# Optimization experiments

Hardware: AMD Instinct MI355X
Metric: run time of the kernel (lower is better)

Reference implementation:

```python
import jax, jax.numpy as jnp
import numpy as np

B, N, E_PER = 32, 2048, 16384
DIN, H = 128, 128
RATIO = 0.3


def setup_inputs() -> dict:
    key = jax.random.key(0)
    ks = jax.random.split(key, 16)
    s_in = 1.0 / np.sqrt(DIN)
    s_h = 1.0 / np.sqrt(H)
    inp = {
        "x": jax.random.normal(ks[0], (B * N, DIN), dtype=jnp.float32),
        "edge_src": jax.random.randint(ks[1], (B, E_PER), 0, N, dtype=jnp.int32),
        "edge_dst": jax.random.randint(ks[2], (B, E_PER), 0, N, dtype=jnp.int32),
        # SAGEConv layer 1: lin_l (neighbor agg, with bias), lin_r (root, no bias)
        "Wl1": jax.random.normal(ks[3], (H, DIN), dtype=jnp.float32) * s_in,
        "bl1": jnp.zeros((H,), dtype=jnp.float32),
        "Wr1": jax.random.normal(ks[4], (H, DIN), dtype=jnp.float32) * s_in,
        # SAGEConv layer 2
        "Wl2": jax.random.normal(ks[5], (H, H), dtype=jnp.float32) * s_h,
        "bl2": jnp.zeros((H,), dtype=jnp.float32),
        "Wr2": jax.random.normal(ks[6], (H, H), dtype=jnp.float32) * s_h,
        # TopKPooling score weight
        "pool_w": jax.random.normal(ks[7], (H,), dtype=jnp.float32) * s_h,
        # classifier MLP
        "Wc1": jax.random.normal(ks[8], (H, H), dtype=jnp.float32) * s_h,
        "bc1": jnp.zeros((H,), dtype=jnp.float32),
        "Wc2": jax.random.normal(ks[9], (1, H), dtype=jnp.float32) * s_h,
        "bc2": jnp.zeros((1,), dtype=jnp.float32),
    }
    return inp


def _sage_conv(x, src, dst, n_total, Wl, bl, Wr):
    # mean-aggregate neighbor messages: msg flows src -> dst
    msg = x[src]                                                   # [E, D] gather
    agg = jax.ops.segment_sum(msg, dst, num_segments=n_total)      # [Nt, D]
    deg = jax.ops.segment_sum(jnp.ones_like(dst, dtype=x.dtype), dst,
                              num_segments=n_total)
    agg = agg / jnp.maximum(deg, 1.0)[:, None]
    return agg @ Wl.T + bl + x @ Wr.T


def _forward(x, edge_src, edge_dst, Wl1, bl1, Wr1, Wl2, bl2, Wr2,
             pool_w, Wc1, bc1, Wc2, bc2):
    n_total = x.shape[0]
    # offset per-graph node ids into the disjoint-union batch
    off = (jnp.arange(B, dtype=edge_src.dtype) * N)[:, None]
    src = (edge_src + off).reshape(-1)
    dst = (edge_dst + off).reshape(-1)

    x = jax.nn.relu(_sage_conv(x, src, dst, n_total, Wl1, bl1, Wr1))
    x = jax.nn.relu(_sage_conv(x, src, dst, n_total, Wl2, bl2, Wr2))

    # TopKPooling: score = tanh(x . w / ||w||); keep top ceil(ratio*N) per graph
    score = jnp.tanh(x @ pool_w / jnp.linalg.norm(pool_w))         # [Nt]
    k = int(np.ceil(RATIO * N))                                    # 615
    vals, idx = jax.lax.top_k(score.reshape(B, N), k)              # [B, k]
    xg = x.reshape(B, N, -1)
    x_sel = jnp.take_along_axis(xg, idx[..., None], axis=1)        # [B, k, H]
    x_sel = x_sel * vals[..., None]                                # gate by score

    # global mean pool over kept nodes, then MLP classifier
    emb = x_sel.mean(axis=1)                                       # [B, H]
    h = jax.nn.relu(emb @ Wc1.T + bc1)
    return (h @ Wc2.T + bc2).squeeze(-1)                           # [B]


def reference(x, edge_src, edge_dst, Wl1, bl1, Wr1, Wl2, bl2, Wr2,
              pool_w, Wc1, bc1, Wc2, bc2):
    return _forward(x, edge_src, edge_dst, Wl1, bl1, Wr1, Wl2, bl2, Wr2,
                    pool_w, Wc1, bc1, Wc2, bc2)
```

## Files before the change

kernel.cpp:

```cpp
#include <hip/hip_runtime.h>
#include <stdint.h>
#include <math.h>

#define NB    32
#define NNODE 2048
#define NT    (NB*NNODE)
#define EPB   16384
#define ETOT  (NB*EPB)
#define DF    128
#define KSEL  615
#define EMAX  512

typedef __attribute__((ext_vector_type(8))) short bf16x8;
typedef __attribute__((ext_vector_type(4))) float f32x4;

__device__ __forceinline__ unsigned short f2bf(float f){
  uint32_t u = __float_as_uint(f);
  u += 0x7FFFu + ((u>>16)&1u);
  return (unsigned short)(u>>16);
}
__device__ __forceinline__ void split2(float f, unsigned short& hi, unsigned short& lo){
  unsigned short h = f2bf(f);
  float fh = __uint_as_float(((uint32_t)h)<<16);
  hi = h;
  lo = f2bf(f - fh);
}
__device__ __forceinline__ uint32_t f2mono(float f){
  uint32_t u = __float_as_uint(f);
  return (u & 0x80000000u) ? ~u : (u | 0x80000000u);
}
__device__ __forceinline__ float mono2f(uint32_t m){
  uint32_t u = (m & 0x80000000u) ? (m ^ 0x80000000u) : ~m;
  return __uint_as_float(u);
}

__global__ void k_deg(const int* __restrict__ edst, uint32_t* __restrict__ deg){
  int e = blockIdx.x*256 + threadIdx.x;
  int g = e >> 14;
  atomicAdd(&deg[g*NNODE + edst[e]], 1u);
}

__global__ __launch_bounds__(1024) void k_scan1(const uint32_t* __restrict__ deg,
                        uint32_t* __restrict__ rowptr, uint32_t* __restrict__ bsum){
  __shared__ uint32_t sh[1024];
  int t = threadIdx.x; int base = blockIdx.x*1024;
  uint32_t v = deg[base+t];
  sh[t] = v;
  for (int off=1; off<1024; off<<=1){
    __syncthreads();
    uint32_t a = (t>=off) ? sh[t-off] : 0u;
    __syncthreads();
    sh[t] += a;
  }
  rowptr[base+t] = sh[t] - v;
  if (t==1023) bsum[blockIdx.x] = sh[1023];
}

__global__ void k_scan2(uint32_t* __restrict__ bsum){
  __shared__ uint32_t sh[64];
  int t = threadIdx.x;
  uint32_t v = bsum[t]; sh[t] = v;
  for (int off=1; off<64; off<<=1){
    __syncthreads();
    uint32_t a = (t>=off) ? sh[t-off] : 0u;
    __syncthreads();
    sh[t] += a;
  }
  bsum[t] = sh[t] - v;
}

__global__ __launch_bounds__(1024) void k_scan3(uint32_t* __restrict__ rowptr,
                                                const uint32_t* __restrict__ bsum){
  int i = blockIdx.x*1024 + threadIdx.x;
  rowptr[i] += bsum[i>>10];
  if (i==0) rowptr[NT] = ETOT;
}

__global__ void k_scatter(const int* __restrict__ esrc, const int* __restrict__ edst,
                          const uint32_t* __restrict__ rowptr, uint32_t* __restrict__ deg,
                          int* __restrict__ col){
  int e = blockIdx.x*256 + threadIdx.x;
  int g = e >> 14;
  int d = g*NNODE + edst[e];
  int s = g*NNODE + esrc[e];
  uint32_t old = atomicSub(&deg[d], 1u);
  col[rowptr[d] + old - 1u] = s;
}

__global__ void k_packB(const float* __restrict__ Wl, const float* __restrict__ Wr,
                        unsigned short* __restrict__ Bpk){
  int t = blockIdx.x*256 + threadIdx.x;
  int lane = t & 63;
  int ct   = (t>>6) & 7;
  int ks   = (t>>9) & 7;
  int c  = ct*16 + (lane & 15);
  int k0 = ks*32 + ((lane>>4)<<3);
  size_t base = ((size_t)((ks*8+ct)*2)*64 + lane)*8;
  #pragma unroll
  for (int j=0;j<8;++j){
    int k = k0 + j;
    float v = (k < DF) ? Wl[c*DF + k] : Wr[c*DF + (k-DF)];
    unsigned short h, l; split2(v, h, l);
    Bpk[base + j]       = h;
    Bpk[base + 512 + j] = l;
  }
}

template<int LAYER>
__global__ __launch_bounds__(128, 4) void k_sage(
    const float* __restrict__ Xin, const uint32_t* __restrict__ rowptr,
    const int* __restrict__ col, const unsigned short* __restrict__ Bpk,
    const float* __restrict__ bias, float* __restrict__ OUT,
    const float* __restrict__ pw, float* __restrict__ scores)
{
  __shared__ float smemA[32][132];
  __shared__ int lcol[EMAX];
  __shared__ uint32_t lrp[33];

  const int t = threadIdx.x;
  const int g = blockIdx.x & 31, jb = blockIdx.x >> 5;
  const int rowBase = g*NNODE + jb*32;

  if (t < 33) lrp[t] = rowptr[rowBase + t];
  const uint32_t e0 = rowptr[rowBase];
  const int ecnt = (int)(rowptr[rowBase + 32] - e0);
  for (int i=t; i<ecnt && i<EMAX; i+=128) lcol[i] = col[e0+i];
  __syncthreads();

  {
    const int grp = t >> 5, c = t & 31;
    const float4* X4 = (const float4*)Xin;
    auto gather = [&](auto colAt){
      for (int n=grp; n<32; n+=4){
        uint32_t b = lrp[n] - e0, e = lrp[n+1] - e0;
        float ax=0.f, ay=0.f, az=0.f, aw=0.f;
        uint32_t k = b;
        for (; k+8<=e; k+=8){
          int s0=colAt(k),  s1=colAt(k+1), s2=colAt(k+2), s3=colAt(k+3),
              s4=colAt(k+4),s5=colAt(k+5), s6=colAt(k+6), s7=colAt(k+7);
          float4 v0=X4[(size_t)s0*32+c], v1=X4[(size_t)s1*32+c],
                 v2=X4[(size_t)s2*32+c], v3=X4[(size_t)s3*32+c],
                 v4=X4[(size_t)s4*32+c], v5=X4[(size_t)s5*32+c],
                 v6=X4[(size_t)s6*32+c], v7=X4[(size_t)s7*32+c];
          ax += ((v0.x+v1.x)+(v2.x+v3.x)) + ((v4.x+v5.x)+(v6.x+v7.x));
          ay += ((v0.y+v1.y)+(v2.y+v3.y)) + ((v4.y+v5.y)+(v6.y+v7.y));
          az += ((v0.z+v1.z)+(v2.z+v3.z)) + ((v4.z+v5.z)+(v6.z+v7.z));
          aw += ((v0.w+v1.w)+(v2.w+v3.w)) + ((v4.w+v5.w)+(v6.w+v7.w));
        }
        for (; k+4<=e; k+=4){
          int s0=colAt(k), s1=colAt(k+1), s2=colAt(k+2), s3=colAt(k+3);
          float4 v0=X4[(size_t)s0*32+c], v1=X4[(size_t)s1*32+c],
                 v2=X4[(size_t)s2*32+c], v3=X4[(size_t)s3*32+c];
          ax += (v0.x+v1.x)+(v2.x+v3.x);
          ay += (v0.y+v1.y)+(v2.y+v3.y);
          az += (v0.z+v1.z)+(v2.z+v3.z);
          aw += (v0.w+v1.w)+(v2.w+v3.w);
        }
        for (; k<e; ++k){
          float4 v = X4[(size_t)colAt(k)*32+c];
          ax+=v.x; ay+=v.y; az+=v.z; aw+=v.w;
        }
        float invd = 1.0f / (float)((e>b)?(e-b):1u);
        *(float4*)&smemA[n][4*c] = make_float4(ax*invd, ay*invd, az*invd, aw*invd);
      }
    };
    if (ecnt <= EMAX) gather([&](uint32_t k){ return lcol[k]; });
    else              gather([&](uint32_t k){ return col[e0+k]; });
  }
  __syncthreads();

  const int l = t & 63, wid = t >> 6;
  const int q = l >> 4, c16 = l & 15;
  const int arow = rowBase + wid*16 + c16;

  f32x4 acc[8];
  #pragma unroll
  for (int ct=0; ct<8; ++ct) acc[ct] = (f32x4){0.f,0.f,0.f,0.f};

  #pragma unroll
  for (int ks=0; ks<8; ++ks){
    float4 A0, A1;
    if (ks < 4){
      const float* s = &smemA[wid*16 + c16][ks*32 + q*8];
      A0 = *(const float4*)s; A1 = *(const float4*)(s+4);
    } else {
      const float* s = Xin + (size_t)arow*DF + (ks-4)*32 + q*8;
      A0 = *(const float4*)s; A1 = *(const float4*)(s+4);
    }
    float v[8] = {A0.x,A0.y,A0.z,A0.w,A1.x,A1.y,A1.z,A1.w};
    bf16x8 ahi, alo;
    #pragma unroll
    for (int j=0;j<8;++j){
      unsigned short h, lo_; split2(v[j], h, lo_);
      ahi[j] = (short)h; alo[j] = (short)lo_;
    }
    const unsigned short* bp = Bpk + (size_t)ks*8192 + l*8;
    #pragma unroll
    for (int ct=0; ct<8; ++ct){
      bf16x8 bhi = *(const bf16x8*)(bp + ct*1024);
      bf16x8 blo = *(const bf16x8*)(bp + ct*1024 + 512);
      acc[ct] = __builtin_amdgcn_mfma_f32_16x16x32_bf16(ahi, bhi, acc[ct], 0,0,0);
      acc[ct] = __builtin_amdgcn_mfma_f32_16x16x32_bf16(ahi, blo, acc[ct], 0,0,0);
      acc[ct] = __builtin_amdgcn_mfma_f32_16x16x32_bf16(alo, bhi, acc[ct], 0,0,0);
    }
  }

  const int rowOut = rowBase + wid*16;
  if constexpr (LAYER==1){
    #pragma unroll
    for (int ct=0; ct<8; ++ct){
      int c = ct*16 + c16;
      float bv = bias[c];
      #pragma unroll
      for (int r=0; r<4; ++r){
        int grow = rowOut + q*4 + r;
        OUT[(size_t)grow*DF + c] = fmaxf(acc[ct][r] + bv, 0.f);
      }
    }
  } else {
    float ov[8][4];
    float pwv[8];
    float n2 = 0.f;
    #pragma unroll
    for (int ct=0; ct<8; ++ct){ pwv[ct] = pw[ct*16 + c16]; n2 += pwv[ct]*pwv[ct]; }
    n2 += __shfl_xor(n2,8,16); n2 += __shfl_xor(n2,4,16);
    n2 += __shfl_xor(n2,2,16); n2 += __shfl_xor(n2,1,16);
    float nrm = sqrtf(n2);
    #pragma unroll
    for (int ct=0; ct<8; ++ct){
      int c = ct*16 + c16;
      float bv = bias[c];
      #pragma unroll
      for (int r=0; r<4; ++r){
        int grow = rowOut + q*4 + r;
        float o = fmaxf(acc[ct][r] + bv, 0.f);
        OUT[(size_t)grow*DF + c] = o;
        ov[ct][r] = o;
      }
    }
    #pragma unroll
    for (int r=0; r<4; ++r){
      float p = 0.f;
      #pragma unroll
      for (int ct=0; ct<8; ++ct) p += ov[ct][r]*pwv[ct];
      p += __shfl_xor(p,8,16); p += __shfl_xor(p,4,16);
      p += __shfl_xor(p,2,16); p += __shfl_xor(p,1,16);
      if (c16 == 0) scores[rowOut + q*4 + r] = tanhf(p/nrm);
    }
  }
}

__global__ __launch_bounds__(1024) void k_topk(
    const float* __restrict__ scores, const float* __restrict__ H,
    const float* __restrict__ Wc1, const float* __restrict__ bc1,
    const float* __restrict__ Wc2, const float* __restrict__ bc2,
    float* __restrict__ out)
{
  __shared__ uint32_t keys[NNODE];
  __shared__ uint32_t hist[64];
  __shared__ uint32_t wsum[16];
  __shared__ uint32_t sh_b, sh_rank, sh_cnt;
  __shared__ unsigned short selidx[KSEL+1];
  __shared__ float selval[KSEL+1];
  __shared__ float part[8*DF];
  __shared__ float emb[DF];
  __shared__ float hred[DF];

  const int t = threadIdx.x; const int b = blockIdx.x;
  const int lane = t & 63, wid = t >> 6;
  const float* sc = scores + b*NNODE;

  for (int i=t; i<NNODE; i+=1024) keys[i] = f2mono(sc[i]);
  __syncthreads();

  uint32_t prefix = 0, prefmask = 0, rank = KSEL, cntT = 0;
  #pragma unroll
  for (int lev=0; lev<6; ++lev){
    const int shift = (lev<5) ? (26 - 6*lev) : 0;
    const uint32_t bmask = (lev<5) ? 63u : 3u;
    if (t < 64) hist[t] = 0;
    __syncthreads();
    for (int i=t; i<NNODE; i+=1024){
      uint32_t k = keys[i];
      if ((k & prefmask) == prefix) atomicAdd(&hist[(k>>shift)&bmask], 1u);
    }
    __syncthreads();
    if (t < 64){
      uint32_t x = hist[t];
      #pragma unroll
      for (int off=1; off<64; off<<=1){
        uint32_t y = __shfl_down(x, off, 64);
        if (t + off < 64) x += y;
      }
      uint32_t above = __shfl_down(x, 1, 64);
      if (t == 63) above = 0;
      if (above < rank && rank <= x){
        sh_b = (uint32_t)t; sh_rank = rank - above; sh_cnt = x - above;
      }
    }
    __syncthreads();
    prefix |= (sh_b << shift);
    prefmask |= (bmask << shift);
    rank = sh_rank; cntT = sh_cnt;
    __syncthreads();
  }
  const uint32_t T = prefix;
  const uint32_t m = rank;

  uint32_t k0 = keys[2*t], k1 = keys[2*t+1];
  uint32_t eq0 = (k0 == T), eq1 = (k1 == T);
  uint32_t eqr0 = 0, eqr1 = 0;

  if (m != cntT){
    uint32_t v = eq0 + eq1, x = v;
    #pragma unroll
    for (int off=1; off<64; off<<=1){
      uint32_t y = __shfl_up(x, off, 64);
      if (lane >= off) x += y;
    }
    if (lane == 63) wsum[wid] = x;
    __syncthreads();
    if (wid == 0){
      uint32_t s = (lane < 16) ? wsum[lane] : 0;
      #pragma unroll
      for (int off=1; off<16; off<<=1){
        uint32_t y = __shfl_up(s, off, 64);
        if (lane >= off) s += y;
      }
      if (lane < 16) wsum[lane] = s;
    }
    __syncthreads();
    uint32_t excl = (wid ? wsum[wid-1] : 0) + x - v;
    eqr0 = excl; eqr1 = excl + eq0;
    __syncthreads();
  }

  uint32_t sel0 = (k0 > T) || (eq0 && eqr0 < m);
  uint32_t sel1 = (k1 > T) || (eq1 && eqr1 < m);
  {
    uint32_t v = sel0 + sel1, x = v;
    #pragma unroll
    for (int off=1; off<64; off<<=1){
      uint32_t y = __shfl_up(x, off, 64);
      if (lane >= off) x += y;
    }
    if (lane == 63) wsum[wid] = x;
    __syncthreads();
    if (wid == 0){
      uint32_t s = (lane < 16) ? wsum[lane] : 0;
      #pragma unroll
      for (int off=1; off<16; off<<=1){
        uint32_t y = __shfl_up(s, off, 64);
        if (lane >= off) s += y;
      }
      if (lane < 16) wsum[lane] = s;
    }
    __syncthreads();
    uint32_t excl = (wid ? wsum[wid-1] : 0) + x - v;
    if (sel0){ selidx[excl] = (unsigned short)(2*t);   selval[excl] = mono2f(k0); }
    if (sel1){ selidx[excl+sel0] = (unsigned short)(2*t+1); selval[excl+sel0] = mono2f(k1); }
  }
  __syncthreads();

  const int pg = t >> 7, f = t & (DF-1);
  const float* Hb = H + (size_t)b*NNODE*DF;
  float accv = 0.f;
  int s2 = pg;
  for (; s2+24 < KSEL; s2 += 32){
    int i0=selidx[s2], i1=selidx[s2+8], i2=selidx[s2+16], i3=selidx[s2+24];
    float w0=selval[s2], w1=selval[s2+8], w2=selval[s2+16], w3=selval[s2+24];
    float v0=Hb[(size_t)i0*DF+f], v1=Hb[(size_t)i1*DF+f],
          v2=Hb[(size_t)i2*DF+f], v3=Hb[(size_t)i3*DF+f];
    accv += w0*v0 + w1*v1 + w2*v2 + w3*v3;
  }
  for (; s2<KSEL; s2+=8) accv += selval[s2]*Hb[(size_t)selidx[s2]*DF+f];
  part[pg*DF + f] = accv;
  __syncthreads();
  if (t < DF){
    float e = 0.f;
    for (int g2=0; g2<8; ++g2) e += part[g2*DF + t];
    emb[t] = e / (float)KSEL;
  }
  __syncthreads();
  if (t < DF){
    float hv = bc1[t];
    const float* wr = Wc1 + t*DF;
    for (int f2=0; f2<DF; ++f2) hv = fmaf(emb[f2], wr[f2], hv);
    hred[t] = fmaxf(hv, 0.f) * Wc2[t];
  }
  __syncthreads();
  if (t == 0){
    float o = bc2[0];
    for (int c2=0; c2<DF; ++c2) o += hred[c2];
    out[b] = o;
  }
}

extern "C" void kernel_launch(void* const* d_in, const int* in_sizes, int n_in,
                              void* d_out, int out_size, void* d_ws, size_t ws_size,
                              hipStream_t stream)
{
  (void)in_sizes; (void)n_in; (void)out_size; (void)ws_size;
  const float* x   = (const float*)d_in[0];
  const int* esrc  = (const int*)d_in[1];
  const int* edst  = (const int*)d_in[2];
  const float* Wl1 = (const float*)d_in[3];
  const float* bl1 = (const float*)d_in[4];
  const float* Wr1 = (const float*)d_in[5];
  const float* Wl2 = (const float*)d_in[6];
  const float* bl2 = (const float*)d_in[7];
  const float* Wr2 = (const float*)d_in[8];
  const float* pw  = (const float*)d_in[9];
  const float* Wc1 = (const float*)d_in[10];
  const float* bc1 = (const float*)d_in[11];
  const float* Wc2 = (const float*)d_in[12];
  const float* bc2 = (const float*)d_in[13];
  float* out = (float*)d_out;

  char* ws = (char*)d_ws;
  float*    H1     = (float*)   (ws + 0);
  float*    H2     = (float*)   (ws + 33554432);
  uint32_t* deg    = (uint32_t*)(ws + 67108864);
  uint32_t* rowptr = (uint32_t*)(ws + 67371008);
  int*      col    = (int*)     (ws + 67633408);
  float*    scores = (float*)   (ws + 69730560);
  uint32_t* bsum   = (uint32_t*)(ws + 69992704);
  unsigned short* Bpk = (unsigned short*)(ws + 69992960);

  hipMemsetAsync(deg, 0, NT*sizeof(uint32_t), stream);

  k_deg    <<<ETOT/256, 256, 0, stream>>>(edst, deg);
  k_scan1  <<<64, 1024, 0, stream>>>(deg, rowptr, bsum);
  k_scan2  <<<1, 64, 0, stream>>>(bsum);
  k_scan3  <<<64, 1024, 0, stream>>>(rowptr, bsum);
  k_scatter<<<ETOT/256, 256, 0, stream>>>(esrc, edst, rowptr, deg, col);

  k_packB<<<16, 256, 0, stream>>>(Wl1, Wr1, Bpk);
  k_packB<<<16, 256, 0, stream>>>(Wl2, Wr2, Bpk + 65536);

  k_sage<1><<<NT/32, 128, 0, stream>>>(x,  rowptr, col, Bpk,         bl1,
                                       H1, nullptr, nullptr);
  k_sage<2><<<NT/32, 128, 0, stream>>>(H1, rowptr, col, Bpk + 65536, bl2,
                                       H2, pw, scores);

  k_topk<<<NB, 1024, 0, stream>>>(scores, H2, Wc1, bc1, Wc2, bc2, out);
}
```

Baseline: 161.3 us.

## Double SAGE block to 256 threads, split output columns across waves, merge packB launches

```diff
diff --git a/kernel.cpp b/kernel.cpp
--- a/kernel.cpp
+++ b/kernel.cpp
@@ -87,9 +87,15 @@
   col[rowptr[d] + old - 1u] = s;
 }
 
-__global__ void k_packB(const float* __restrict__ Wl, const float* __restrict__ Wr,
+__global__ void k_packB(const float* __restrict__ Wl1, const float* __restrict__ Wr1,
+                        const float* __restrict__ Wl2, const float* __restrict__ Wr2,
                         unsigned short* __restrict__ Bpk){
-  int t = blockIdx.x*256 + threadIdx.x;
+  int tt = blockIdx.x*256 + threadIdx.x;
+  int layer = tt >> 12;
+  int t = tt & 4095;
+  const float* Wl = layer ? Wl2 : Wl1;
+  const float* Wr = layer ? Wr2 : Wr1;
+  unsigned short* B = Bpk + (size_t)layer*65536;
   int lane = t & 63;
   int ct   = (t>>6) & 7;
   int ks   = (t>>9) & 7;
@@ -101,13 +107,13 @@
     int k = k0 + j;
     float v = (k < DF) ? Wl[c*DF + k] : Wr[c*DF + (k-DF)];
     unsigned short h, l; split2(v, h, l);
-    Bpk[base + j]       = h;
-    Bpk[base + 512 + j] = l;
+    B[base + j]       = h;
+    B[base + 512 + j] = l;
   }
 }
 
 template<int LAYER>
-__global__ __launch_bounds__(128, 4) void k_sage(
+__global__ __launch_bounds__(256, 4) void k_sage(
     const float* __restrict__ Xin, const uint32_t* __restrict__ rowptr,
     const int* __restrict__ col, const unsigned short* __restrict__ Bpk,
     const float* __restrict__ bias, float* __restrict__ OUT,
@@ -116,6 +122,8 @@
   __shared__ float smemA[32][132];
   __shared__ int lcol[EMAX];
   __shared__ uint32_t lrp[33];
+  __shared__ float sp_p[32][2];
+  __shared__ float sp_n2[2];
 
   const int t = threadIdx.x;
   const int g = blockIdx.x & 31, jb = blockIdx.x >> 5;
@@ -124,14 +132,27 @@
   if (t < 33) lrp[t] = rowptr[rowBase + t];
   const uint32_t e0 = rowptr[rowBase];
   const int ecnt = (int)(rowptr[rowBase + 32] - e0);
-  for (int i=t; i<ecnt && i<EMAX; i+=128) lcol[i] = col[e0+i];
+  for (int i=t; i<ecnt && i<EMAX; i+=256) lcol[i] = col[e0+i];
+
+  const int l = t & 63, wid = t >> 6;
+  const int q = l >> 4, c16 = l & 15;
+  const int rhalf = wid & 1, cthalf = wid >> 1;
+  const int arow = rowBase + rhalf*16 + c16;
+
+  float4 own[8];
+  #pragma unroll
+  for (int ks4=0; ks4<4; ++ks4){
+    const float* s = Xin + (size_t)arow*DF + ks4*32 + q*8;
+    own[ks4*2]   = *(const float4*)s;
+    own[ks4*2+1] = *(const float4*)(s+4);
+  }
   __syncthreads();
 
   {
     const int grp = t >> 5, c = t & 31;
     const float4* X4 = (const float4*)Xin;
     auto gather = [&](auto colAt){
-      for (int n=grp; n<32; n+=4){
+      for (int n=grp; n<32; n+=8){
         uint32_t b = lrp[n] - e0, e = lrp[n+1] - e0;
         float ax=0.f, ay=0.f, az=0.f, aw=0.f;
         uint32_t k = b;
@@ -169,23 +190,18 @@
   }
   __syncthreads();
 
-  const int l = t & 63, wid = t >> 6;
-  const int q = l >> 4, c16 = l & 15;
-  const int arow = rowBase + wid*16 + c16;
-
-  f32x4 acc[8];
+  f32x4 acc[4];
   #pragma unroll
-  for (int ct=0; ct<8; ++ct) acc[ct] = (f32x4){0.f,0.f,0.f,0.f};
+  for (int ct=0; ct<4; ++ct) acc[ct] = (f32x4){0.f,0.f,0.f,0.f};
 
   #pragma unroll
   for (int ks=0; ks<8; ++ks){
     float4 A0, A1;
     if (ks < 4){
-      const float* s = &smemA[wid*16 + c16][ks*32 + q*8];
+      const float* s = &smemA[rhalf*16 + c16][ks*32 + q*8];
       A0 = *(const float4*)s; A1 = *(const float4*)(s+4);
     } else {
-      const float* s = Xin + (size_t)arow*DF + (ks-4)*32 + q*8;
-      A0 = *(const float4*)s; A1 = *(const float4*)(s+4);
+      A0 = own[(ks-4)*2]; A1 = own[(ks-4)*2+1];
     }
     float v[8] = {A0.x,A0.y,A0.z,A0.w,A1.x,A1.y,A1.z,A1.w};
     bf16x8 ahi, alo;
@@ -194,9 +210,9 @@
       unsigned short h, lo_; split2(v[j], h, lo_);
       ahi[j] = (short)h; alo[j] = (short)lo_;
     }
-    const unsigned short* bp = Bpk + (size_t)ks*8192 + l*8;
-    #pragma unroll
-    for (int ct=0; ct<8; ++ct){
+    const unsigned short* bp = Bpk + (size_t)ks*8192 + (size_t)cthalf*4096 + l*8;
+    #pragma unroll
+    for (int ct=0; ct<4; ++ct){
       bf16x8 bhi = *(const bf16x8*)(bp + ct*1024);
       bf16x8 blo = *(const bf16x8*)(bp + ct*1024 + 512);
       acc[ct] = __builtin_amdgcn_mfma_f32_16x16x32_bf16(ahi, bhi, acc[ct], 0,0,0);
@@ -205,11 +221,11 @@
     }
   }
 
-  const int rowOut = rowBase + wid*16;
+  const int rowOut = rowBase + rhalf*16;
   if constexpr (LAYER==1){
     #pragma unroll
-    for (int ct=0; ct<8; ++ct){
-      int c = ct*16 + c16;
+    for (int ct=0; ct<4; ++ct){
+      int c = cthalf*64 + ct*16 + c16;
       float bv = bias[c];
       #pragma unroll
       for (int r=0; r<4; ++r){
@@ -218,17 +234,20 @@
       }
     }
   } else {
-    float ov[8][4];
-    float pwv[8];
+    float ov[4][4];
+    float pwv[4];
     float n2 = 0.f;
     #pragma unroll
-    for (int ct=0; ct<8; ++ct){ pwv[ct] = pw[ct*16 + c16]; n2 += pwv[ct]*pwv[ct]; }
+    for (int ct=0; ct<4; ++ct){
+      pwv[ct] = pw[cthalf*64 + ct*16 + c16];
+      n2 += pwv[ct]*pwv[ct];
+    }
     n2 += __shfl_xor(n2,8,16); n2 += __shfl_xor(n2,4,16);
     n2 += __shfl_xor(n2,2,16); n2 += __shfl_xor(n2,1,16);
-    float nrm = sqrtf(n2);
-    #pragma unroll
-    for (int ct=0; ct<8; ++ct){
-      int c = ct*16 + c16;
+    if (l == 0) sp_n2[cthalf] = n2;
+    #pragma unroll
+    for (int ct=0; ct<4; ++ct){
+      int c = cthalf*64 + ct*16 + c16;
       float bv = bias[c];
       #pragma unroll
       for (int r=0; r<4; ++r){
@@ -242,10 +261,16 @@
     for (int r=0; r<4; ++r){
       float p = 0.f;
       #pragma unroll
-      for (int ct=0; ct<8; ++ct) p += ov[ct][r]*pwv[ct];
+      for (int ct=0; ct<4; ++ct) p += ov[ct][r]*pwv[ct];
       p += __shfl_xor(p,8,16); p += __shfl_xor(p,4,16);
       p += __shfl_xor(p,2,16); p += __shfl_xor(p,1,16);
-      if (c16 == 0) scores[rowOut + q*4 + r] = tanhf(p/nrm);
+      if (c16 == 0) sp_p[rhalf*16 + q*4 + r][cthalf] = p;
+    }
+    __syncthreads();
+    if (t < 32){
+      float p = sp_p[t][0] + sp_p[t][1];
+      float nrm = sqrtf(sp_n2[0] + sp_n2[1]);
+      scores[rowBase + t] = tanhf(p/nrm);
     }
   }
 }
@@ -435,12 +460,11 @@
   k_scan3  <<<64, 1024, 0, stream>>>(rowptr, bsum);
   k_scatter<<<ETOT/256, 256, 0, stream>>>(esrc, edst, rowptr, deg, col);
 
-  k_packB<<<16, 256, 0, stream>>>(Wl1, Wr1, Bpk);
-  k_packB<<<16, 256, 0, stream>>>(Wl2, Wr2, Bpk + 65536);
-
-  k_sage<1><<<NT/32, 128, 0, stream>>>(x,  rowptr, col, Bpk,         bl1,
+  k_packB<<<32, 256, 0, stream>>>(Wl1, Wr1, Wl2, Wr2, Bpk);
+
+  k_sage<1><<<NT/32, 256, 0, stream>>>(x,  rowptr, col, Bpk,         bl1,
                                        H1, nullptr, nullptr);
-  k_sage<2><<<NT/32, 128, 0, stream>>>(H1, rowptr, col, Bpk + 65536, bl2,
+  k_sage<2><<<NT/32, 256, 0, stream>>>(H1, rowptr, col, Bpk + 65536, bl2,
                                        H2, pw, scores);
 
   k_topk<<<NB, 1024, 0, stream>>>(scores, H2, Wc1, bc1, Wc2, bc2, out);
```

Measured after the change: 168.3 us. 1.04x slower.

## Fuse CSR build and weight packing into one per-graph LDS kernel

Applied to the files above, without the earlier changes.

```diff
diff --git a/kernel.cpp b/kernel.cpp
--- a/kernel.cpp
+++ b/kernel.cpp
@@ -33,76 +33,92 @@
   uint32_t u = (m & 0x80000000u) ? (m ^ 0x80000000u) : ~m;
   return __uint_as_float(u);
 }
-
-__global__ void k_deg(const int* __restrict__ edst, uint32_t* __restrict__ deg){
-  int e = blockIdx.x*256 + threadIdx.x;
-  int g = e >> 14;
-  atomicAdd(&deg[g*NNODE + edst[e]], 1u);
-}
-
-__global__ __launch_bounds__(1024) void k_scan1(const uint32_t* __restrict__ deg,
-                        uint32_t* __restrict__ rowptr, uint32_t* __restrict__ bsum){
-  __shared__ uint32_t sh[1024];
-  int t = threadIdx.x; int base = blockIdx.x*1024;
-  uint32_t v = deg[base+t];
-  sh[t] = v;
-  for (int off=1; off<1024; off<<=1){
-    __syncthreads();
-    uint32_t a = (t>=off) ? sh[t-off] : 0u;
-    __syncthreads();
-    sh[t] += a;
-  }
-  rowptr[base+t] = sh[t] - v;
-  if (t==1023) bsum[blockIdx.x] = sh[1023];
-}
-
-__global__ void k_scan2(uint32_t* __restrict__ bsum){
-  __shared__ uint32_t sh[64];
-  int t = threadIdx.x;
-  uint32_t v = bsum[t]; sh[t] = v;
-  for (int off=1; off<64; off<<=1){
-    __syncthreads();
-    uint32_t a = (t>=off) ? sh[t-off] : 0u;
-    __syncthreads();
-    sh[t] += a;
-  }
-  bsum[t] = sh[t] - v;
-}
-
-__global__ __launch_bounds__(1024) void k_scan3(uint32_t* __restrict__ rowptr,
-                                                const uint32_t* __restrict__ bsum){
-  int i = blockIdx.x*1024 + threadIdx.x;
-  rowptr[i] += bsum[i>>10];
-  if (i==0) rowptr[NT] = ETOT;
-}
-
-__global__ void k_scatter(const int* __restrict__ esrc, const int* __restrict__ edst,
-                          const uint32_t* __restrict__ rowptr, uint32_t* __restrict__ deg,
-                          int* __restrict__ col){
-  int e = blockIdx.x*256 + threadIdx.x;
-  int g = e >> 14;
-  int d = g*NNODE + edst[e];
-  int s = g*NNODE + esrc[e];
-  uint32_t old = atomicSub(&deg[d], 1u);
-  col[rowptr[d] + old - 1u] = s;
-}
-
-__global__ void k_packB(const float* __restrict__ Wl, const float* __restrict__ Wr,
-                        unsigned short* __restrict__ Bpk){
-  int t = blockIdx.x*256 + threadIdx.x;
-  int lane = t & 63;
-  int ct   = (t>>6) & 7;
-  int ks   = (t>>9) & 7;
-  int c  = ct*16 + (lane & 15);
-  int k0 = ks*32 + ((lane>>4)<<3);
-  size_t base = ((size_t)((ks*8+ct)*2)*64 + lane)*8;
-  #pragma unroll
-  for (int j=0;j<8;++j){
-    int k = k0 + j;
-    float v = (k < DF) ? Wl[c*DF + k] : Wr[c*DF + (k-DF)];
-    unsigned short h, l; split2(v, h, l);
-    Bpk[base + j]       = h;
-    Bpk[base + 512 + j] = l;
+__device__ __forceinline__ f32x4 ntload4(const float* p){
+  return __builtin_nontemporal_load((const f32x4*)p);
+}
+__device__ __forceinline__ void ntstore(float v, float* p){
+  __builtin_nontemporal_store(v, p);
+}
+
+__global__ __launch_bounds__(256) void k_prep(
+    const int* __restrict__ esrc, const int* __restrict__ edst,
+    const float* __restrict__ Wl1, const float* __restrict__ Wr1,
+    const float* __restrict__ Wl2, const float* __restrict__ Wr2,
+    uint32_t* __restrict__ rowptr, int* __restrict__ col,
+    unsigned short* __restrict__ Bpk)
+{
+  __shared__ uint32_t hist[NNODE];
+  __shared__ uint32_t wsum4[4];
+  const int t = threadIdx.x;
+  const int bid = blockIdx.x;
+
+  if (bid < NB){
+    const int g = bid;
+    const int lane = t & 63, wid = t >> 6;
+    for (int i=t; i<NNODE; i+=256) hist[i] = 0;
+    __syncthreads();
+    const int* ed = edst + g*EPB;
+    const int* es = esrc + g*EPB;
+    for (int e=t; e<EPB; e+=256) atomicAdd(&hist[ed[e]], 1u);
+    __syncthreads();
+    uint32_t v0,v1,v2,v3,v4,v5,v6,v7;
+    const int b8 = t*8;
+    v0=hist[b8+0]; v1=hist[b8+1]; v2=hist[b8+2]; v3=hist[b8+3];
+    v4=hist[b8+4]; v5=hist[b8+5]; v6=hist[b8+6]; v7=hist[b8+7];
+    uint32_t tsum = v0+v1+v2+v3+v4+v5+v6+v7;
+    uint32_t x = tsum;
+    #pragma unroll
+    for (int off=1; off<64; off<<=1){
+      uint32_t y = __shfl_up(x, off, 64);
+      if (lane >= off) x += y;
+    }
+    if (lane == 63) wsum4[wid] = x;
+    __syncthreads();
+    if (t == 0){
+      uint32_t a = 0;
+      #pragma unroll
+      for (int w=0; w<4; ++w){ uint32_t tmp=wsum4[w]; wsum4[w]=a; a+=tmp; }
+    }
+    __syncthreads();
+    uint32_t run = wsum4[wid] + x - tsum;
+    uint32_t* rp = rowptr + g*NNODE + b8;
+    uint32_t h;
+    h=v0; hist[b8+0]=run; rp[0]=g*EPB+run; run+=h;
+    h=v1; hist[b8+1]=run; rp[1]=g*EPB+run; run+=h;
+    h=v2; hist[b8+2]=run; rp[2]=g*EPB+run; run+=h;
+    h=v3; hist[b8+3]=run; rp[3]=g*EPB+run; run+=h;
+    h=v4; hist[b8+4]=run; rp[4]=g*EPB+run; run+=h;
+    h=v5; hist[b8+5]=run; rp[5]=g*EPB+run; run+=h;
+    h=v6; hist[b8+6]=run; rp[6]=g*EPB+run; run+=h;
+    h=v7; hist[b8+7]=run; rp[7]=g*EPB+run; run+=h;
+    if (g == 0 && t == 0) rowptr[NT] = ETOT;
+    __syncthreads();
+    for (int e=t; e<EPB; e+=256){
+      int d = ed[e];
+      uint32_t slot = atomicAdd(&hist[d], 1u);
+      col[g*EPB + slot] = g*NNODE + es[e];
+    }
+  } else {
+    int tt = (bid - NB)*256 + t;
+    int layer = tt >> 12;
+    int t2 = tt & 4095;
+    const float* Wl = layer ? Wl2 : Wl1;
+    const float* Wr = layer ? Wr2 : Wr1;
+    unsigned short* B = Bpk + (size_t)layer*65536;
+    int lane = t2 & 63;
+    int ct   = (t2>>6) & 7;
+    int ks   = (t2>>9) & 7;
+    int c  = ct*16 + (lane & 15);
+    int k0 = ks*32 + ((lane>>4)<<3);
+    size_t base = ((size_t)((ks*8+ct)*2)*64 + lane)*8;
+    #pragma unroll
+    for (int j=0;j<8;++j){
+      int k = k0 + j;
+      float v = (k < DF) ? Wl[c*DF + k] : Wr[c*DF + (k-DF)];
+      unsigned short h, l; split2(v, h, l);
+      B[base + j]       = h;
+      B[base + 512 + j] = l;
+    }
   }
 }
 
@@ -125,43 +141,46 @@
   const uint32_t e0 = rowptr[rowBase];
   const int ecnt = (int)(rowptr[rowBase + 32] - e0);
   for (int i=t; i<ecnt && i<EMAX; i+=128) lcol[i] = col[e0+i];
+
+  const int l = t & 63, wid = t >> 6;
+  const int q = l >> 4, c16 = l & 15;
+  const int arow = rowBase + wid*16 + c16;
+  f32x4 own[8];
+  #pragma unroll
+  for (int ks4=0; ks4<4; ++ks4){
+    const float* s = Xin + (size_t)arow*DF + ks4*32 + q*8;
+    own[ks4*2]   = ntload4(s);
+    own[ks4*2+1] = ntload4(s+4);
+  }
   __syncthreads();
 
   {
     const int grp = t >> 5, c = t & 31;
-    const float4* X4 = (const float4*)Xin;
     auto gather = [&](auto colAt){
       for (int n=grp; n<32; n+=4){
         uint32_t b = lrp[n] - e0, e = lrp[n+1] - e0;
-        float ax=0.f, ay=0.f, az=0.f, aw=0.f;
+        f32x4 a = {0.f,0.f,0.f,0.f};
         uint32_t k = b;
         for (; k+8<=e; k+=8){
           int s0=colAt(k),  s1=colAt(k+1), s2=colAt(k+2), s3=colAt(k+3),
               s4=colAt(k+4),s5=colAt(k+5), s6=colAt(k+6), s7=colAt(k+7);
-          float4 v0=X4[(size_t)s0*32+c], v1=X4[(size_t)s1*32+c],
-                 v2=X4[(size_t)s2*32+c], v3=X4[(size_t)s3*32+c],
-                 v4=X4[(size_t)s4*32+c], v5=X4[(size_t)s5*32+c],
-                 v6=X4[(size_t)s6*32+c], v7=X4[(size_t)s7*32+c];
-          ax += ((v0.x+v1.x)+(v2.x+v3.x)) + ((v4.x+v5.x)+(v6.x+v7.x));
-          ay += ((v0.y+v1.y)+(v2.y+v3.y)) + ((v4.y+v5.y)+(v6.y+v7.y));
-          az += ((v0.z+v1.z)+(v2.z+v3.z)) + ((v4.z+v5.z)+(v6.z+v7.z));
-          aw += ((v0.w+v1.w)+(v2.w+v3.w)) + ((v4.w+v5.w)+(v6.w+v7.w));
+          f32x4 v0=ntload4(Xin+(size_t)s0*DF+4*c), v1=ntload4(Xin+(size_t)s1*DF+4*c),
+                v2=ntload4(Xin+(size_t)s2*DF+4*c), v3=ntload4(Xin+(size_t)s3*DF+4*c),
+                v4=ntload4(Xin+(size_t)s4*DF+4*c), v5=ntload4(Xin+(size_t)s5*DF+4*c),
+                v6=ntload4(Xin+(size_t)s6*DF+4*c), v7=ntload4(Xin+(size_t)s7*DF+4*c);
+          a += ((v0+v1)+(v2+v3)) + ((v4+v5)+(v6+v7));
         }
         for (; k+4<=e; k+=4){
           int s0=colAt(k), s1=colAt(k+1), s2=colAt(k+2), s3=colAt(k+3);
-          float4 v0=X4[(size_t)s0*32+c], v1=X4[(size_t)s1*32+c],
-                 v2=X4[(size_t)s2*32+c], v3=X4[(size_t)s3*32+c];
-          ax += (v0.x+v1.x)+(v2.x+v3.x);
-          ay += (v0.y+v1.y)+(v2.y+v3.y);
-          az += (v0.z+v1.z)+(v2.z+v3.z);
-          aw += (v0.w+v1.w)+(v2.w+v3.w);
+          f32x4 v0=ntload4(Xin+(size_t)s0*DF+4*c), v1=ntload4(Xin+(size_t)s1*DF+4*c),
+                v2=ntload4(Xin+(size_t)s2*DF+4*c), v3=ntload4(Xin+(size_t)s3*DF+4*c);
+          a += (v0+v1)+(v2+v3);
         }
         for (; k<e; ++k){
-          float4 v = X4[(size_t)colAt(k)*32+c];
-          ax+=v.x; ay+=v.y; az+=v.z; aw+=v.w;
+          a += ntload4(Xin+(size_t)colAt(k)*DF+4*c);
         }
         float invd = 1.0f / (float)((e>b)?(e-b):1u);
-        *(float4*)&smemA[n][4*c] = make_float4(ax*invd, ay*invd, az*invd, aw*invd);
+        *(f32x4*)&smemA[n][4*c] = a * invd;
       }
     };
     if (ecnt <= EMAX) gather([&](uint32_t k){ return lcol[k]; });
@@ -169,23 +188,18 @@
   }
   __syncthreads();
 
-  const int l = t & 63, wid = t >> 6;
-  const int q = l >> 4, c16 = l & 15;
-  const int arow = rowBase + wid*16 + c16;
-
   f32x4 acc[8];
   #pragma unroll
   for (int ct=0; ct<8; ++ct) acc[ct] = (f32x4){0.f,0.f,0.f,0.f};
 
   #pragma unroll
   for (int ks=0; ks<8; ++ks){
-    float4 A0, A1;
+    f32x4 A0, A1;
     if (ks < 4){
       const float* s = &smemA[wid*16 + c16][ks*32 + q*8];
-      A0 = *(const float4*)s; A1 = *(const float4*)(s+4);
+      A0 = *(const f32x4*)s; A1 = *(const f32x4*)(s+4);
     } else {
-      const float* s = Xin + (size_t)arow*DF + (ks-4)*32 + q*8;
-      A0 = *(const float4*)s; A1 = *(const float4*)(s+4);
+      A0 = own[(ks-4)*2]; A1 = own[(ks-4)*2+1];
     }
     float v[8] = {A0.x,A0.y,A0.z,A0.w,A1.x,A1.y,A1.z,A1.w};
     bf16x8 ahi, alo;
@@ -214,7 +228,7 @@
       #pragma unroll
       for (int r=0; r<4; ++r){
         int grow = rowOut + q*4 + r;
-        OUT[(size_t)grow*DF + c] = fmaxf(acc[ct][r] + bv, 0.f);
+        ntstore(fmaxf(acc[ct][r] + bv, 0.f), &OUT[(size_t)grow*DF + c]);
       }
     }
   } else {
@@ -234,7 +248,7 @@
       for (int r=0; r<4; ++r){
         int grow = rowOut + q*4 + r;
         float o = fmaxf(acc[ct][r] + bv, 0.f);
-        OUT[(size_t)grow*DF + c] = o;
+        ntstore(o, &OUT[(size_t)grow*DF + c]);
         ov[ct][r] = o;
       }
     }
@@ -420,23 +434,13 @@
   char* ws = (char*)d_ws;
   float*    H1     = (float*)   (ws + 0);
   float*    H2     = (float*)   (ws + 33554432);
-  uint32_t* deg    = (uint32_t*)(ws + 67108864);
-  uint32_t* rowptr = (uint32_t*)(ws + 67371008);
-  int*      col    = (int*)     (ws + 67633408);
-  float*    scores = (float*)   (ws + 69730560);
-  uint32_t* bsum   = (uint32_t*)(ws + 69992704);
-  unsigned short* Bpk = (unsigned short*)(ws + 69992960);
-
-  hipMemsetAsync(deg, 0, NT*sizeof(uint32_t), stream);
-
-  k_deg    <<<ETOT/256, 256, 0, stream>>>(edst, deg);
-  k_scan1  <<<64, 1024, 0, stream>>>(deg, rowptr, bsum);
-  k_scan2  <<<1, 64, 0, stream>>>(bsum);
-  k_scan3  <<<64, 1024, 0, stream>>>(rowptr, bsum);
-  k_scatter<<<ETOT/256, 256, 0, stream>>>(esrc, edst, rowptr, deg, col);
-
-  k_packB<<<16, 256, 0, stream>>>(Wl1, Wr1, Bpk);
-  k_packB<<<16, 256, 0, stream>>>(Wl2, Wr2, Bpk + 65536);
+  uint32_t* rowptr = (uint32_t*)(ws + 67108864);
+  int*      col    = (int*)     (ws + 67371264);
+  float*    scores = (float*)   (ws + 69468416);
+  unsigned short* Bpk = (unsigned short*)(ws + 69730560);
+
+  k_prep<<<64, 256, 0, stream>>>(esrc, edst, Wl1, Wr1, Wl2, Wr2,
+                                 rowptr, col, Bpk);
 
   k_sage<1><<<NT/32, 128, 0, stream>>>(x,  rowptr, col, Bpk,         bl1,
                                        H1, nullptr, nullptr);
```

Measured after the change: 165.8 us. 1.03x slower.

## Fuse weight packing into degree kernel, prefetch own rows, use nontemporal loads/stores

Applied to the files above, without the earlier changes.

```diff
diff --git a/kernel.cpp b/kernel.cpp
--- a/kernel.cpp
+++ b/kernel.cpp
@@ -33,11 +33,44 @@
   uint32_t u = (m & 0x80000000u) ? (m ^ 0x80000000u) : ~m;
   return __uint_as_float(u);
 }
-
-__global__ void k_deg(const int* __restrict__ edst, uint32_t* __restrict__ deg){
-  int e = blockIdx.x*256 + threadIdx.x;
-  int g = e >> 14;
-  atomicAdd(&deg[g*NNODE + edst[e]], 1u);
+__device__ __forceinline__ f32x4 ntload4(const float* p){
+  return __builtin_nontemporal_load((const f32x4*)p);
+}
+__device__ __forceinline__ void ntstore(float v, float* p){
+  __builtin_nontemporal_store(v, p);
+}
+
+__global__ void k_deg(const int* __restrict__ edst, uint32_t* __restrict__ deg,
+                      const float* __restrict__ Wl1, const float* __restrict__ Wr1,
+                      const float* __restrict__ Wl2, const float* __restrict__ Wr2,
+                      unsigned short* __restrict__ Bpk){
+  const int bid = blockIdx.x;
+  if (bid < ETOT/256){
+    int e = bid*256 + threadIdx.x;
+    int g = e >> 14;
+    atomicAdd(&deg[g*NNODE + edst[e]], 1u);
+  } else {
+    int tt = (bid - ETOT/256)*256 + threadIdx.x;
+    int layer = tt >> 12;
+    int t2 = tt & 4095;
+    const float* Wl = layer ? Wl2 : Wl1;
+    const float* Wr = layer ? Wr2 : Wr1;
+    unsigned short* B = Bpk + (size_t)layer*65536;
+    int lane = t2 & 63;
+    int ct   = (t2>>6) & 7;
+    int ks   = (t2>>9) & 7;
+    int c  = ct*16 + (lane & 15);
+    int k0 = ks*32 + ((lane>>4)<<3);
+    size_t base = ((size_t)((ks*8+ct)*2)*64 + lane)*8;
+    #pragma unroll
+    for (int j=0;j<8;++j){
+      int k = k0 + j;
+      float v = (k < DF) ? Wl[c*DF + k] : Wr[c*DF + (k-DF)];
+      unsigned short h, l; split2(v, h, l);
+      B[base + j]       = h;
+      B[base + 512 + j] = l;
+    }
+  }
 }
 
 __global__ __launch_bounds__(1024) void k_scan1(const uint32_t* __restrict__ deg,
@@ -85,25 +118,6 @@
   int s = g*NNODE + esrc[e];
   uint32_t old = atomicSub(&deg[d], 1u);
   col[rowptr[d] + old - 1u] = s;
-}
-
-__global__ void k_packB(const float* __restrict__ Wl, const float* __restrict__ Wr,
-                        unsigned short* __restrict__ Bpk){
-  int t = blockIdx.x*256 + threadIdx.x;
-  int lane = t & 63;
-  int ct   = (t>>6) & 7;
-  int ks   = (t>>9) & 7;
-  int c  = ct*16 + (lane & 15);
-  int k0 = ks*32 + ((lane>>4)<<3);
-  size_t base = ((size_t)((ks*8+ct)*2)*64 + lane)*8;
-  #pragma unroll
-  for (int j=0;j<8;++j){
-    int k = k0 + j;
-    float v = (k < DF) ? Wl[c*DF + k] : Wr[c*DF + (k-DF)];
-    unsigned short h, l; split2(v, h, l);
-    Bpk[base + j]       = h;
-    Bpk[base + 512 + j] = l;
-  }
 }
 
 template<int LAYER>
@@ -125,43 +139,46 @@
   const uint32_t e0 = rowptr[rowBase];
   const int ecnt = (int)(rowptr[rowBase + 32] - e0);
   for (int i=t; i<ecnt && i<EMAX; i+=128) lcol[i] = col[e0+i];
+
+  const int l = t & 63, wid = t >> 6;
+  const int q = l >> 4, c16 = l & 15;
+  const int arow = rowBase + wid*16 + c16;
+  f32x4 own[8];
+  #pragma unroll
+  for (int ks4=0; ks4<4; ++ks4){
+    const float* s = Xin + (size_t)arow*DF + ks4*32 + q*8;
+    own[ks4*2]   = ntload4(s);
+    own[ks4*2+1] = ntload4(s+4);
+  }
   __syncthreads();
 
   {
     const int grp = t >> 5, c = t & 31;
-    const float4* X4 = (const float4*)Xin;
     auto gather = [&](auto colAt){
       for (int n=grp; n<32; n+=4){
         uint32_t b = lrp[n] - e0, e = lrp[n+1] - e0;
-        float ax=0.f, ay=0.f, az=0.f, aw=0.f;
+        f32x4 a = {0.f,0.f,0.f,0.f};
         uint32_t k = b;
         for (; k+8<=e; k+=8){
           int s0=colAt(k),  s1=colAt(k+1), s2=colAt(k+2), s3=colAt(k+3),
               s4=colAt(k+4),s5=colAt(k+5), s6=colAt(k+6), s7=colAt(k+7);
-          float4 v0=X4[(size_t)s0*32+c], v1=X4[(size_t)s1*32+c],
-                 v2=X4[(size_t)s2*32+c], v3=X4[(size_t)s3*32+c],
-                 v4=X4[(size_t)s4*32+c], v5=X4[(size_t)s5*32+c],
-                 v6=X4[(size_t)s6*32+c], v7=X4[(size_t)s7*32+c];
-          ax += ((v0.x+v1.x)+(v2.x+v3.x)) + ((v4.x+v5.x)+(v6.x+v7.x));
-          ay += ((v0.y+v1.y)+(v2.y+v3.y)) + ((v4.y+v5.y)+(v6.y+v7.y));
-          az += ((v0.z+v1.z)+(v2.z+v3.z)) + ((v4.z+v5.z)+(v6.z+v7.z));
-          aw += ((v0.w+v1.w)+(v2.w+v3.w)) + ((v4.w+v5.w)+(v6.w+v7.w));
+          f32x4 v0=ntload4(Xin+(size_t)s0*DF+4*c), v1=ntload4(Xin+(size_t)s1*DF+4*c),
+                v2=ntload4(Xin+(size_t)s2*DF+4*c), v3=ntload4(Xin+(size_t)s3*DF+4*c),
+                v4=ntload4(Xin+(size_t)s4*DF+4*c), v5=ntload4(Xin+(size_t)s5*DF+4*c),
+                v6=ntload4(Xin+(size_t)s6*DF+4*c), v7=ntload4(Xin+(size_t)s7*DF+4*c);
+          a += ((v0+v1)+(v2+v3)) + ((v4+v5)+(v6+v7));
         }
         for (; k+4<=e; k+=4){
           int s0=colAt(k), s1=colAt(k+1), s2=colAt(k+2), s3=colAt(k+3);
-          float4 v0=X4[(size_t)s0*32+c], v1=X4[(size_t)s1*32+c],
-                 v2=X4[(size_t)s2*32+c], v3=X4[(size_t)s3*32+c];
-          ax += (v0.x+v1.x)+(v2.x+v3.x);
-          ay += (v0.y+v1.y)+(v2.y+v3.y);
-          az += (v0.z+v1.z)+(v2.z+v3.z);
-          aw += (v0.w+v1.w)+(v2.w+v3.w);
+          f32x4 v0=ntload4(Xin+(size_t)s0*DF+4*c), v1=ntload4(Xin+(size_t)s1*DF+4*c),
+                v2=ntload4(Xin+(size_t)s2*DF+4*c), v3=ntload4(Xin+(size_t)s3*DF+4*c);
+          a += (v0+v1)+(v2+v3);
         }
         for (; k<e; ++k){
-          float4 v = X4[(size_t)colAt(k)*32+c];
-          ax+=v.x; ay+=v.y; az+=v.z; aw+=v.w;
+          a += ntload4(Xin+(size_t)colAt(k)*DF+4*c);
         }
         float invd = 1.0f / (float)((e>b)?(e-b):1u);
-        *(float4*)&smemA[n][4*c] = make_float4(ax*invd, ay*invd, az*invd, aw*invd);
+        *(f32x4*)&smemA[n][4*c] = a * invd;
       }
     };
     if (ecnt <= EMAX) gather([&](uint32_t k){ return lcol[k]; });
@@ -169,23 +186,18 @@
   }
   __syncthreads();
 
-  const int l = t & 63, wid = t >> 6;
-  const int q = l >> 4, c16 = l & 15;
-  const int arow = rowBase + wid*16 + c16;
-
   f32x4 acc[8];
   #pragma unroll
   for (int ct=0; ct<8; ++ct) acc[ct] = (f32x4){0.f,0.f,0.f,0.f};
 
   #pragma unroll
   for (int ks=0; ks<8; ++ks){
-    float4 A0, A1;
+    f32x4 A0, A1;
     if (ks < 4){
       const float* s = &smemA[wid*16 + c16][ks*32 + q*8];
-      A0 = *(const float4*)s; A1 = *(const float4*)(s+4);
+      A0 = *(const f32x4*)s; A1 = *(const f32x4*)(s+4);
     } else {
-      const float* s = Xin + (size_t)arow*DF + (ks-4)*32 + q*8;
-      A0 = *(const float4*)s; A1 = *(const float4*)(s+4);
+      A0 = own[(ks-4)*2]; A1 = own[(ks-4)*2+1];
     }
     float v[8] = {A0.x,A0.y,A0.z,A0.w,A1.x,A1.y,A1.z,A1.w};
     bf16x8 ahi, alo;
@@ -214,7 +226,7 @@
       #pragma unroll
       for (int r=0; r<4; ++r){
         int grow = rowOut + q*4 + r;
-        OUT[(size_t)grow*DF + c] = fmaxf(acc[ct][r] + bv, 0.f);
+        ntstore(fmaxf(acc[ct][r] + bv, 0.f), &OUT[(size_t)grow*DF + c]);
       }
     }
   } else {
@@ -234,7 +246,7 @@
       for (int r=0; r<4; ++r){
         int grow = rowOut + q*4 + r;
         float o = fmaxf(acc[ct][r] + bv, 0.f);
-        OUT[(size_t)grow*DF + c] = o;
+        ntstore(o, &OUT[(size_t)grow*DF + c]);
         ov[ct][r] = o;
       }
     }
@@ -429,15 +441,12 @@
 
   hipMemsetAsync(deg, 0, NT*sizeof(uint32_t), stream);
 
-  k_deg    <<<ETOT/256, 256, 0, stream>>>(edst, deg);
+  k_deg    <<<ETOT/256 + 32, 256, 0, stream>>>(edst, deg, Wl1, Wr1, Wl2, Wr2, Bpk);
   k_scan1  <<<64, 1024, 0, stream>>>(deg, rowptr, bsum);
   k_scan2  <<<1, 64, 0, stream>>>(bsum);
   k_scan3  <<<64, 1024, 0, stream>>>(rowptr, bsum);
   k_scatter<<<ETOT/256, 256, 0, stream>>>(esrc, edst, rowptr, deg, col);
 
-  k_packB<<<16, 256, 0, stream>>>(Wl1, Wr1, Bpk);
-  k_packB<<<16, 256, 0, stream>>>(Wl2, Wr2, Bpk + 65536);
-
   k_sage<1><<<NT/32, 128, 0, stream>>>(x,  rowptr, col, Bpk,         bl1,
                                        H1, nullptr, nullptr);
   k_sage<2><<<NT/32, 128, 0, stream>>>(H1, rowptr, col, Bpk + 65536, bl2,
```

Result: slower. 184.4 us (+14.3%).
